# Kernel tuning notes

Measured on AMD Instinct MI355X. Metric: run time of the kernel, lower is better.

## Reference

```python
import jax, jax.numpy as jnp
import numpy as np
from jax import lax

B, H_IMG, W_IMG = 512, 812, 40
HID = 128
NUM_CLASSES = 12
LSTM_IN = 32 * ((W_IMG - 5) // 2 + 1)  # 32 channels * 18 = 576


def setup_inputs() -> dict:
    key = jax.random.key(0)
    ks = jax.random.split(key, 20)
    s = 0.05
    inp = {
        "x": jax.random.normal(ks[0], (B, 1, H_IMG, W_IMG), jnp.float32),
        "conv_w": jax.random.normal(ks[1], (32, 1, 20, 5), jnp.float32) * s,
        "conv_b": jax.random.normal(ks[2], (32,), jnp.float32) * s,
        "Wih0": jax.random.normal(ks[3], (4 * HID, LSTM_IN), jnp.float32) * s,
        "Whh0": jax.random.normal(ks[4], (4 * HID, HID), jnp.float32) * s,
        "bih0": jax.random.normal(ks[5], (4 * HID,), jnp.float32) * s,
        "bhh0": jax.random.normal(ks[6], (4 * HID,), jnp.float32) * s,
        "Wih1": jax.random.normal(ks[7], (4 * HID, HID), jnp.float32) * s,
        "Whh1": jax.random.normal(ks[8], (4 * HID, HID), jnp.float32) * s,
        "bih1": jax.random.normal(ks[9], (4 * HID,), jnp.float32) * s,
        "bhh1": jax.random.normal(ks[10], (4 * HID,), jnp.float32) * s,
        "W_att": jax.random.normal(ks[11], (HID, HID), jnp.float32) * s,
        "b_att": jax.random.normal(ks[12], (HID,), jnp.float32) * s,
        "v_att": jax.random.normal(ks[13], (HID,), jnp.float32) * s,
        "W1": jax.random.normal(ks[14], (64, HID), jnp.float32) * s,
        "b1": jax.random.normal(ks[15], (64,), jnp.float32) * s,
        "W2": jax.random.normal(ks[16], (NUM_CLASSES, 64), jnp.float32) * s,
        "b2": jax.random.normal(ks[17], (NUM_CLASSES,), jnp.float32) * s,
    }
    return inp


def _lstm_layer(seq, Wih, Whh, bih, bhh):
    # seq: (T, B, I); PyTorch gate order i, f, g, o
    T, Bn, _ = seq.shape
    Hd = Whh.shape[1]
    x_proj = jnp.einsum('tbi,gi->tbg', seq, Wih) + bih + bhh  # (T,B,4H)

    def step(carry, xg):
        h, c = carry
        g = xg + h @ Whh.T
        i, f, gg, o = jnp.split(g, 4, axis=-1)
        c = jax.nn.sigmoid(f) * c + jax.nn.sigmoid(i) * jnp.tanh(gg)
        h = jax.nn.sigmoid(o) * jnp.tanh(c)
        return (h, c), h

    init = (jnp.zeros((Bn, Hd), seq.dtype), jnp.zeros((Bn, Hd), seq.dtype))
    _, hs = lax.scan(step, init, x_proj)
    return hs  # (T,B,H)


def _forward(x, conv_w, conv_b, Wih0, Whh0, bih0, bhh0, Wih1, Whh1, bih1, bhh1,
             W_att, b_att, v_att, W1, b1, W2, b2):
    # Conv2d(1->32, k=(20,5), s=(8,2)) + ReLU
    y = lax.conv_general_dilated(x, conv_w, (8, 2), 'VALID',
                                 dimension_numbers=('NCHW', 'OIHW', 'NCHW'))
    y = jax.nn.relu(y + conv_b[None, :, None, None])  # (B,32,T,W')
    b, c, t, w = y.shape
    # permute(0,2,3,1).view(b,t,-1).permute(1,0,2) -> (T,B,W'*32)
    seq = jnp.transpose(y, (2, 0, 3, 1)).reshape(t, b, w * c)
    # 2-layer LSTM (inter-layer dropout=0.2 inactive at eval)
    h1 = _lstm_layer(seq, Wih0, Whh0, bih0, bhh0)
    h2 = _lstm_layer(h1, Wih1, Whh1, bih1, bhh1)
    # additive attention pooling over time
    squish = jnp.tanh(jnp.einsum('tbh,hk->tbk', h2, W_att) + b_att)  # (T,B,H)
    attn = jnp.einsum('tbh,h->tb', squish, v_att)                     # (T,B)
    w_att_n = jax.nn.softmax(attn, axis=0)                            # softmax over T
    pooled = jnp.einsum('tb,tbh->bh', w_att_n, h2)                    # (B,H)
    # dnn1 -> (dropout inactive at eval) -> output
    hdn = pooled @ W1.T + b1
    return hdn @ W2.T + b2  # (B,num_classes)


def reference(x, conv_w, conv_b, Wih0, Whh0, bih0, bhh0, Wih1, Whh1, bih1, bhh1,
              W_att, b_att, v_att, W1, b1, W2, b2):
    return _forward(x, conv_w, conv_b, Wih0, Whh0, bih0, bhh0, Wih1, Whh1,
                    bih1, bhh1, W_att, b_att, v_att, W1, b1, W2, b2)
```

## Files before the change

kernel.cpp:

```cpp
#include <hip/hip_runtime.h>
#include <stdint.h>


#define T_STEPS 100
#define BATCH   512
#define HIDD    128
#define GATES   512
#define LSTMIN  576
#define HIMG    812
#define WIMG    40

typedef __attribute__((ext_vector_type(8))) short bf16x8;
typedef __attribute__((ext_vector_type(4))) float f32x4;
typedef __attribute__((ext_vector_type(2))) __fp16 f16x2;
typedef unsigned long long ull;

__device__ inline unsigned short f2bf(float f) {
  unsigned u = __float_as_uint(f);
  unsigned r = (u + 0x7fffu + ((u >> 16) & 1u)) >> 16;
  return (unsigned short)r;
}
__device__ inline unsigned pk_bf16(float a, float b) {
#if __has_builtin(__builtin_amdgcn_cvt_pk_bf16_f32)
  auto r = __builtin_amdgcn_cvt_pk_bf16_f32(a, b);
  return __builtin_bit_cast(unsigned, r);
#else
  return (unsigned)f2bf(a) | ((unsigned)f2bf(b) << 16);
#endif
}
__device__ inline float bf2f(unsigned short b) {
  return __uint_as_float(((unsigned)b) << 16);
}
__device__ inline float fsigm(float x) {
  float e = __expf(-x);
  return __builtin_amdgcn_rcpf(1.f + e);
}
__device__ inline float ftanh(float x) {
  float e = __expf(2.f * x);
  return (e - 1.f) * __builtin_amdgcn_rcpf(e + 1.f);
}
__device__ inline void lds_barrier() {
  asm volatile("s_waitcnt lgkmcnt(0)" ::: "memory");
  __builtin_amdgcn_s_barrier();
}
__device__ inline void wait_flag(int* fp, int need) {
  if ((threadIdx.x & 63) == 0) {
    while (__hip_atomic_load(fp, __ATOMIC_RELAXED, __HIP_MEMORY_SCOPE_AGENT) < need)
      __builtin_amdgcn_s_sleep(2);
  }
  asm volatile("" ::: "memory");
}

__global__ void prep_kernel(const float* __restrict__ Wih0, const float* __restrict__ Whh0,
                            const float* __restrict__ Wih1, const float* __restrict__ Whh1,
                            const float* __restrict__ Watt, const float* __restrict__ convw,
                            const float* __restrict__ bih0, const float* __restrict__ bhh0,
                            const float* __restrict__ bih1, const float* __restrict__ bhh1,
                            unsigned short* __restrict__ wih0b, unsigned short* __restrict__ whh0b,
                            unsigned short* __restrict__ wih1b, unsigned short* __restrict__ whh1b,
                            unsigned short* __restrict__ wattb, f16x2* __restrict__ wpair,
                            float* __restrict__ bias0, float* __restrict__ bias1,
                            int* __restrict__ flags) {
  int tid = blockIdx.x * blockDim.x + threadIdx.x;
  int stride = gridDim.x * blockDim.x;
  for (int i = tid; i < GATES * LSTMIN; i += stride) wih0b[i] = f2bf(Wih0[i]);
  for (int i = tid; i < GATES * HIDD; i += stride) whh0b[i] = f2bf(Whh0[i]);
  for (int i = tid; i < GATES * HIDD; i += stride) wih1b[i] = f2bf(Wih1[i]);
  for (int i = tid; i < GATES * HIDD; i += stride) whh1b[i] = f2bf(Whh1[i]);
  for (int i = tid; i < HIDD * HIDD; i += stride) {
    int j = i >> 7, k = i & 127;
    wattb[i] = f2bf(Watt[k * HIDD + j]);
  }
  for (int i = tid; i < 50 * 32; i += stride) {
    int k2 = i >> 5, c = i & 31;
    int kh2 = k2 / 5, kw = k2 % 5;
    float lo = convw[c * 100 + (2 * kh2) * 5 + kw];
    float hi = convw[c * 100 + (2 * kh2 + 1) * 5 + kw];
    wpair[i] = __builtin_amdgcn_cvt_pkrtz(lo, hi);
  }
  for (int i = tid; i < GATES; i += stride) bias0[i] = bih0[i] + bhh0[i];
  for (int i = tid; i < GATES; i += stride) bias1[i] = bih1[i] + bhh1[i];
  for (int i = tid; i < 32; i += stride) flags[i] = 0;
}

__global__ __launch_bounds__(256) void conv_kernel(const float* __restrict__ x,
                                                   const f16x2* __restrict__ wpair,
                                                   const float* __restrict__ convb,
                                                   unsigned short* __restrict__ seq) {
  __shared__ f16x2 imgp[106 * WIMG];
  const int b = blockIdx.x;
  const int chunk = blockIdx.y;
  const int t0 = chunk * 25;
  const float* src = x + (size_t)b * (HIMG * WIMG) + (size_t)(8 * t0) * WIMG;
  for (int i = threadIdx.x; i < 106 * WIMG; i += 256) {
    int r2 = i / WIMG, c = i % WIMG;
    float lo = src[(2 * r2) * WIMG + c];
    float hi = src[(2 * r2 + 1) * WIMG + c];
    imgp[i] = __builtin_amdgcn_cvt_pkrtz(lo, hi);
  }
  __syncthreads();
  for (int p = threadIdx.x; p < 450; p += 256) {
    int tl = p / 18, wp = p % 18;
    int t = t0 + tl;
    float acc[32];
#pragma unroll
    for (int c = 0; c < 32; ++c) acc[c] = 0.f;
    const f16x2* ibase = imgp + (4 * tl) * WIMG + 2 * wp;
#pragma unroll 2
    for (int kh2 = 0; kh2 < 10; ++kh2) {
#pragma unroll
      for (int kw = 0; kw < 5; ++kw) {
        f16x2 iv = ibase[kh2 * WIMG + kw];
        const f16x2* wk = wpair + (kh2 * 5 + kw) * 32;
#pragma unroll
        for (int c = 0; c < 32; ++c)
          acc[c] = __builtin_amdgcn_fdot2(iv, wk[c], acc[c], false);
      }
    }
    unsigned short* o = seq + ((size_t)(t * BATCH + b)) * LSTMIN + wp * 32;
#pragma unroll
    for (int c = 0; c < 32; ++c) {
      float v = acc[c] + convb[c];
      o[c] = f2bf(v > 0.f ? v : 0.f);
    }
  }
}

template <int KDIM>
__global__ __launch_bounds__(256) void gemm_xp_kernel(const unsigned short* __restrict__ A,
                                                      const unsigned short* __restrict__ Bw,
                                                      const float* __restrict__ bias,
                                                      unsigned short* __restrict__ Xp) {
  __shared__ __align__(16) unsigned short As[128 * 32];
  __shared__ __align__(16) unsigned short Bs[128 * 32];
  const int tid = threadIdx.x;
  const int lane = tid & 63;
  const int w = tid >> 6;
  const int col16 = lane & 15;
  const int q = lane >> 4;
  const int n0 = blockIdx.x * 128;
  const int m0 = blockIdx.y * 128;
  const int wm = (w & 1) * 64;
  const int wn = (w >> 1) * 64;
  f32x4 acc[4][4] = {};
  const int r = tid >> 2;
  const int sw = ((tid & 3) ^ (r & 3)) * 8;
  const unsigned wslot = (unsigned)w * 512;
  const unsigned short* ga = A + (size_t)(m0 + r) * KDIM + sw;
  const unsigned short* gb = Bw + (size_t)(n0 + r) * KDIM + sw;
  for (int k0 = 0; k0 < KDIM; k0 += 32) {
    __syncthreads();
    __builtin_amdgcn_global_load_lds((const __attribute__((address_space(1))) void*)(ga + k0),
                                     (__attribute__((address_space(3))) void*)(As + wslot), 16, 0, 0);
    __builtin_amdgcn_global_load_lds((const __attribute__((address_space(1))) void*)(ga + k0 + (size_t)64 * KDIM),
                                     (__attribute__((address_space(3))) void*)(As + wslot + 2048), 16, 0, 0);
    __builtin_amdgcn_global_load_lds((const __attribute__((address_space(1))) void*)(gb + k0),
                                     (__attribute__((address_space(3))) void*)(Bs + wslot), 16, 0, 0);
    __builtin_amdgcn_global_load_lds((const __attribute__((address_space(1))) void*)(gb + k0 + (size_t)64 * KDIM),
                                     (__attribute__((address_space(3))) void*)(Bs + wslot + 2048), 16, 0, 0);
    __syncthreads();
    bf16x8 af[4], bv[4];
#pragma unroll
    for (int i = 0; i < 4; ++i) {
      int ra = wm + i * 16 + col16;
      af[i] = *(const bf16x8*)(As + ra * 32 + ((q ^ (ra & 3)) * 8));
      int rb2 = wn + i * 16 + col16;
      bv[i] = *(const bf16x8*)(Bs + rb2 * 32 + ((q ^ (rb2 & 3)) * 8));
    }
#pragma unroll
    for (int i = 0; i < 4; ++i)
#pragma unroll
      for (int j = 0; j < 4; ++j)
        acc[i][j] = __builtin_amdgcn_mfma_f32_16x16x32_bf16(af[i], bv[j], acc[i][j], 0, 0, 0);
  }
#pragma unroll
  for (int ct = 0; ct < 4; ++ct) {
    int n = n0 + wn + ct * 16 + col16;
    float bvv = bias[n];
    int g = n >> 7;
    int rr2 = n & 127;
    int wqS = rr2 >> 5;
    int ntS = g * 2 + ((rr2 >> 4) & 1);
    int c16S = n & 15;
#pragma unroll
    for (int rt = 0; rt < 4; ++rt) {
      int m = m0 + wm + rt * 16 + q * 4;
      int t = m >> 9;
      int bb = m & 511;
      int blkS = bb >> 4;
      int r16 = bb & 15;
      ushort4 u;
      u.x = f2bf(acc[rt][ct][0] + bvv);
      u.y = f2bf(acc[rt][ct][1] + bvv);
      u.z = f2bf(acc[rt][ct][2] + bvv);
      u.w = f2bf(acc[rt][ct][3] + bvv);
      size_t tile = (((size_t)t * 32 + blkS) * 4 + wqS) * 8 + ntS;
      *(ushort4*)(Xp + tile * 256 + c16S * 16 + r16) = u;
    }
  }
}

__global__ __launch_bounds__(512, 2) void scan_pipe_kernel(
    const unsigned short* __restrict__ Xp0, const unsigned short* __restrict__ Whh0,
    const unsigned short* __restrict__ Wih1, const float* __restrict__ bias1,
    unsigned short* __restrict__ Xp1, const unsigned short* __restrict__ Whh1,
    unsigned short* __restrict__ hout, int* __restrict__ flags) {
  __shared__ __align__(16) unsigned short hb[2][16 * 136];
  const int tid = threadIdx.x;
  const int lane = tid & 63;
  const int w = tid >> 6;
  const int wq = w & 3;
  const int role = w >> 2;
  const int col16 = lane & 15;
  const int q = lane >> 4;
  const bool producer = blockIdx.x < 32;
  const int blk = producer ? (int)blockIdx.x : (int)blockIdx.x - 32;
  const int rb = blk * 16;
  int* flagp = flags + blk;
  const size_t TSTRIDE = (size_t)GATES * BATCH;
  const size_t TSTRIDE8 = TSTRIDE / 4;

  {
    unsigned short* hz = (unsigned short*)hb;
    for (int i = tid; i < 2 * 16 * 136; i += 512) hz[i] = 0;
  }

  if (producer) {
    if (role == 0) {
      bf16x8 bfrag[8][4];
      const unsigned short* xpb[8];
#pragma unroll
      for (int nt = 0; nt < 8; ++nt) {
        int cn = (nt >> 1) * HIDD + wq * 32 + (nt & 1) * 16 + col16;
#pragma unroll
        for (int ks = 0; ks < 4; ++ks)
          bfrag[nt][ks] = *(const bf16x8*)(Whh0 + (size_t)cn * HIDD + ks * 32 + q * 8);
        size_t tile = (((size_t)blk) * 4 + wq) * 8 + nt;
        xpb[nt] = Xp0 + tile * 256 + col16 * 16 + q * 4;
      }
      uint2 xb[2][8];
#pragma unroll
      for (int nt = 0; nt < 8; ++nt) xb[0][nt] = *(const uint2*)(xpb[nt]);
#pragma unroll
      for (int nt = 0; nt < 8; ++nt) xb[1][nt] = *(const uint2*)(xpb[nt] + TSTRIDE);
      float cst[8] = {0.f, 0.f, 0.f, 0.f, 0.f, 0.f, 0.f, 0.f};
      lds_barrier();
#pragma unroll 2
      for (int t = 0; t < T_STEPS; ++t) {
        const int s = t & 1;
        uint2 xv[8];
#pragma unroll
        for (int nt = 0; nt < 8; ++nt) xv[nt] = xb[s][nt];
        if (t + 2 < T_STEPS) {
#pragma unroll
          for (int nt = 0; nt < 8; ++nt)
            xb[s][nt] = *(const uint2*)(xpb[nt] + (size_t)(t + 2) * TSTRIDE);
        }
        bf16x8 af[4];
#pragma unroll
        for (int ks = 0; ks < 4; ++ks)
          af[ks] = *(const bf16x8*)(hb[s ^ 1] + col16 * 136 + ks * 32 + q * 8);
        f32x4 acc[8];
#pragma unroll
        for (int nt = 0; nt < 8; ++nt) {
          acc[nt][0] = __uint_as_float(xv[nt].x << 16);
          acc[nt][1] = __uint_as_float(xv[nt].x & 0xffff0000u);
          acc[nt][2] = __uint_as_float(xv[nt].y << 16);
          acc[nt][3] = __uint_as_float(xv[nt].y & 0xffff0000u);
        }
#pragma unroll
        for (int ks = 0; ks < 4; ++ks)
#pragma unroll
          for (int nt = 0; nt < 8; ++nt)
            acc[nt] = __builtin_amdgcn_mfma_f32_16x16x32_bf16(af[ks], bfrag[nt][ks], acc[nt], 0, 0, 0);
#pragma unroll
        for (int hh = 0; hh < 2; ++hh)
#pragma unroll
          for (int rr = 0; rr < 4; ++rr) {
            int idx = hh * 4 + rr;
            float pi = acc[0 + hh][rr];
            float pf = acc[2 + hh][rr];
            float pg = acc[4 + hh][rr];
            float po = acc[6 + hh][rr];
            float cc = fsigm(pf) * cst[idx] + fsigm(pi) * ftanh(pg);
            cst[idx] = cc;
            hb[s][(q * 4 + rr) * 136 + wq * 32 + hh * 16 + col16] = f2bf(fsigm(po) * ftanh(cc));
          }
        lds_barrier();
      }
      lds_barrier();
    } else {
      bf16x8 bfrag2[8][4];
      float biasn[8];
      ull* xob[8];
#pragma unroll
      for (int nt = 0; nt < 8; ++nt) {
        int cn = (nt >> 1) * HIDD + wq * 32 + (nt & 1) * 16 + col16;
#pragma unroll
        for (int ks = 0; ks < 4; ++ks)
          bfrag2[nt][ks] = *(const bf16x8*)(Wih1 + (size_t)cn * HIDD + ks * 32 + q * 8);
        biasn[nt] = bias1[cn];
        size_t tile = (((size_t)blk) * 4 + wq) * 8 + nt;
        xob[nt] = (ull*)(Xp1 + tile * 256 + col16 * 16 + q * 4);
      }
      lds_barrier();
#pragma unroll 2
      for (int t = 0; t < T_STEPS; ++t) {
        const int s = t & 1;
        if (t > 0) {
          bf16x8 af[4];
#pragma unroll
          for (int ks = 0; ks < 4; ++ks)
            af[ks] = *(const bf16x8*)(hb[s ^ 1] + col16 * 136 + ks * 32 + q * 8);
          f32x4 acc2[8];
#pragma unroll
          for (int nt = 0; nt < 8; ++nt) acc2[nt] = f32x4{0.f, 0.f, 0.f, 0.f};
#pragma unroll
          for (int ks = 0; ks < 4; ++ks)
#pragma unroll
            for (int nt = 0; nt < 8; ++nt)
              acc2[nt] = __builtin_amdgcn_mfma_f32_16x16x32_bf16(af[ks], bfrag2[nt][ks], acc2[nt], 0, 0, 0);
#pragma unroll
          for (int nt = 0; nt < 8; ++nt) {
            unsigned lo = pk_bf16(acc2[nt][0] + biasn[nt], acc2[nt][1] + biasn[nt]);
            unsigned hi = pk_bf16(acc2[nt][2] + biasn[nt], acc2[nt][3] + biasn[nt]);
            __hip_atomic_store(xob[nt] + (size_t)(t - 1) * TSTRIDE8,
                               (ull)lo | ((ull)hi << 32),
                               __ATOMIC_RELAXED, __HIP_MEMORY_SCOPE_AGENT);
          }
        }
        if ((t & 3) == 3) {
          asm volatile("s_waitcnt vmcnt(0) lgkmcnt(0)\ns_barrier" ::: "memory");
          if (tid == 256)
            __hip_atomic_store(flagp, t, __ATOMIC_RELAXED, __HIP_MEMORY_SCOPE_AGENT);
        } else {
          lds_barrier();
        }
      }
      {
        bf16x8 af[4];
#pragma unroll
        for (int ks = 0; ks < 4; ++ks)
          af[ks] = *(const bf16x8*)(hb[(T_STEPS - 1) & 1] + col16 * 136 + ks * 32 + q * 8);
        f32x4 acc2[8];
#pragma unroll
        for (int nt = 0; nt < 8; ++nt) acc2[nt] = f32x4{0.f, 0.f, 0.f, 0.f};
#pragma unroll
        for (int ks = 0; ks < 4; ++ks)
#pragma unroll
          for (int nt = 0; nt < 8; ++nt)
            acc2[nt] = __builtin_amdgcn_mfma_f32_16x16x32_bf16(af[ks], bfrag2[nt][ks], acc2[nt], 0, 0, 0);
#pragma unroll
        for (int nt = 0; nt < 8; ++nt) {
          unsigned lo = pk_bf16(acc2[nt][0] + biasn[nt], acc2[nt][1] + biasn[nt]);
          unsigned hi = pk_bf16(acc2[nt][2] + biasn[nt], acc2[nt][3] + biasn[nt]);
          __hip_atomic_store(xob[nt] + (size_t)(T_STEPS - 1) * TSTRIDE8,
                             (ull)lo | ((ull)hi << 32),
                             __ATOMIC_RELAXED, __HIP_MEMORY_SCOPE_AGENT);
        }
        asm volatile("s_waitcnt vmcnt(0) lgkmcnt(0)\ns_barrier" ::: "memory");
        if (tid == 256)
          __hip_atomic_store(flagp, 100, __ATOMIC_RELAXED, __HIP_MEMORY_SCOPE_AGENT);
      }
    }
  } else {
    if (role == 0) {
      bf16x8 bfrag[8][4];
      ull* xpb[8];
#pragma unroll
      for (int nt = 0; nt < 8; ++nt) {
        int cn = (nt >> 1) * HIDD + wq * 32 + (nt & 1) * 16 + col16;
#pragma unroll
        for (int ks = 0; ks < 4; ++ks)
          bfrag[nt][ks] = *(const bf16x8*)(Whh1 + (size_t)cn * HIDD + ks * 32 + q * 8);
        size_t tile = (((size_t)blk) * 4 + wq) * 8 + nt;
        xpb[nt] = (ull*)(Xp1 + tile * 256 + col16 * 16 + q * 4);
      }
      wait_flag(flagp, 6);
      ull xb[2][8];
#pragma unroll
      for (int nt = 0; nt < 8; ++nt)
        xb[0][nt] = __hip_atomic_load(xpb[nt], __ATOMIC_RELAXED, __HIP_MEMORY_SCOPE_AGENT);
#pragma unroll
      for (int nt = 0; nt < 8; ++nt)
        xb[1][nt] = __hip_atomic_load(xpb[nt] + TSTRIDE8, __ATOMIC_RELAXED, __HIP_MEMORY_SCOPE_AGENT);
      float cst[8] = {0.f, 0.f, 0.f, 0.f, 0.f, 0.f, 0.f, 0.f};
      lds_barrier();
#pragma unroll 2
      for (int t = 0; t < T_STEPS; ++t) {
        if (t > 0 && (t & 3) == 0) {
          int need = t + 6;
          if (need > 100) need = 100;
          wait_flag(flagp, need);
        }
        const int s = t & 1;
        ull xv[8];
#pragma unroll
        for (int nt = 0; nt < 8; ++nt) xv[nt] = xb[s][nt];
        if (t + 2 < T_STEPS) {
#pragma unroll
          for (int nt = 0; nt < 8; ++nt)
            xb[s][nt] = __hip_atomic_load(xpb[nt] + (size_t)(t + 2) * TSTRIDE8,
                                          __ATOMIC_RELAXED, __HIP_MEMORY_SCOPE_AGENT);
        }
        bf16x8 af[4];
#pragma unroll
        for (int ks = 0; ks < 4; ++ks)
          af[ks] = *(const bf16x8*)(hb[s ^ 1] + col16 * 136 + ks * 32 + q * 8);
        f32x4 acc[8];
#pragma unroll
        for (int nt = 0; nt < 8; ++nt) {
          unsigned lo = (unsigned)xv[nt];
          unsigned hi = (unsigned)(xv[nt] >> 32);
          acc[nt][0] = __uint_as_float(lo << 16);
          acc[nt][1] = __uint_as_float(lo & 0xffff0000u);
          acc[nt][2] = __uint_as_float(hi << 16);
          acc[nt][3] = __uint_as_float(hi & 0xffff0000u);
        }
#pragma unroll
        for (int ks = 0; ks < 4; ++ks)
#pragma unroll
          for (int nt = 0; nt < 8; ++nt)
            acc[nt] = __builtin_amdgcn_mfma_f32_16x16x32_bf16(af[ks], bfrag[nt][ks], acc[nt], 0, 0, 0);
#pragma unroll
        for (int hh = 0; hh < 2; ++hh)
#pragma unroll
          for (int rr = 0; rr < 4; ++rr) {
            int idx = hh * 4 + rr;
            float pi = acc[0 + hh][rr];
            float pf = acc[2 + hh][rr];
            float pg = acc[4 + hh][rr];
            float po = acc[6 + hh][rr];
            float cc = fsigm(pf) * cst[idx] + fsigm(pi) * ftanh(pg);
            cst[idx] = cc;
            hb[s][(q * 4 + rr) * 136 + wq * 32 + hh * 16 + col16] = f2bf(fsigm(po) * ftanh(cc));
          }
        lds_barrier();
      }
    } else {
      const int c = wq * 64 + lane;
      const int row = c >> 4;
      const int ch = c & 15;
      lds_barrier();
#pragma unroll 2
      for (int t = 0; t < T_STEPS; ++t) {
        if (t > 0) {
          uint4 hx = *(const uint4*)(hb[(t - 1) & 1] + row * 136 + ch * 8);
          *(uint4*)(hout + ((size_t)((t - 1) * BATCH) + rb + row) * HIDD + ch * 8) = hx;
        }
        lds_barrier();
      }
      uint4 hx = *(const uint4*)(hb[(T_STEPS - 1) & 1] + row * 136 + ch * 8);
      *(uint4*)(hout + ((size_t)((T_STEPS - 1) * BATCH) + rb + row) * HIDD + ch * 8) = hx;
    }
  }
}

__global__ __launch_bounds__(256) void gemm_att_kernel(const unsigned short* __restrict__ A,
                                                       const unsigned short* __restrict__ Bw,
                                                       const float* __restrict__ b_att,
                                                       const float* __restrict__ v_att,
                                                       float* __restrict__ scores) {
  __shared__ __align__(16) unsigned short As[128 * 32];
  __shared__ __align__(16) unsigned short Bs[128 * 32];
  __shared__ float s_red[128];
  const int tid = threadIdx.x;
  const int lane = tid & 63;
  const int w = tid >> 6;
  const int col16 = lane & 15;
  const int q = lane >> 4;
  const int m0 = blockIdx.y * 128;
  const int wm = (w & 1) * 64;
  const int wn = (w >> 1) * 64;
  f32x4 acc[4][4] = {};
  const int r = tid >> 2;
  const int sw = ((tid & 3) ^ (r & 3)) * 8;
  const unsigned wslot = (unsigned)w * 512;
  const unsigned short* ga = A + (size_t)(m0 + r) * HIDD + sw;
  const unsigned short* gb = Bw + (size_t)r * HIDD + sw;
  for (int k0 = 0; k0 < HIDD; k0 += 32) {
    __syncthreads();
    __builtin_amdgcn_global_load_lds((const __attribute__((address_space(1))) void*)(ga + k0),
                                     (__attribute__((address_space(3))) void*)(As + wslot), 16, 0, 0);
    __builtin_amdgcn_global_load_lds((const __attribute__((address_space(1))) void*)(ga + k0 + (size_t)64 * HIDD),
                                     (__attribute__((address_space(3))) void*)(As + wslot + 2048), 16, 0, 0);
    __builtin_amdgcn_global_load_lds((const __attribute__((address_space(1))) void*)(gb + k0),
                                     (__attribute__((address_space(3))) void*)(Bs + wslot), 16, 0, 0);
    __builtin_amdgcn_global_load_lds((const __attribute__((address_space(1))) void*)(gb + k0 + (size_t)64 * HIDD),
                                     (__attribute__((address_space(3))) void*)(Bs + wslot + 2048), 16, 0, 0);
    __syncthreads();
    bf16x8 af[4], bv[4];
#pragma unroll
    for (int i = 0; i < 4; ++i) {
      int ra = wm + i * 16 + col16;
      af[i] = *(const bf16x8*)(As + ra * 32 + ((q ^ (ra & 3)) * 8));
      int rb2 = wn + i * 16 + col16;
      bv[i] = *(const bf16x8*)(Bs + rb2 * 32 + ((q ^ (rb2 & 3)) * 8));
    }
#pragma unroll
    for (int i = 0; i < 4; ++i)
#pragma unroll
      for (int j = 0; j < 4; ++j)
        acc[i][j] = __builtin_amdgcn_mfma_f32_16x16x32_bf16(af[i], bv[j], acc[i][j], 0, 0, 0);
  }
  if (tid < 128) s_red[tid] = 0.f;
  float rs[4][4];
#pragma unroll
  for (int rt = 0; rt < 4; ++rt)
#pragma unroll
    for (int rr = 0; rr < 4; ++rr) rs[rt][rr] = 0.f;
#pragma unroll
  for (int ct = 0; ct < 4; ++ct) {
    int n = wn + ct * 16 + col16;
    float bvv = b_att[n], vv = v_att[n];
#pragma unroll
    for (int rt = 0; rt < 4; ++rt)
#pragma unroll
      for (int rr = 0; rr < 4; ++rr) {
        float xv2 = acc[rt][ct][rr] + bvv;
        float e = __expf(2.f * xv2);
        rs[rt][rr] += vv * (e - 1.f) * __builtin_amdgcn_rcpf(e + 1.f);
      }
  }
#pragma unroll
  for (int off = 1; off < 16; off <<= 1)
#pragma unroll
    for (int rt = 0; rt < 4; ++rt)
#pragma unroll
      for (int rr = 0; rr < 4; ++rr) rs[rt][rr] += __shfl_xor(rs[rt][rr], off, 64);
  __syncthreads();
  if (col16 == 0) {
#pragma unroll
    for (int rt = 0; rt < 4; ++rt)
#pragma unroll
      for (int rr = 0; rr < 4; ++rr)
        atomicAdd(&s_red[wm + rt * 16 + q * 4 + rr], rs[rt][rr]);
  }
  __syncthreads();
  if (tid < 128) scores[m0 + tid] = s_red[tid];
}

__global__ __launch_bounds__(128) void final_kernel(const float* __restrict__ scores,
                                                    const unsigned short* __restrict__ h2,
                                                    const float* __restrict__ W1, const float* __restrict__ b1,
                                                    const float* __restrict__ W2, const float* __restrict__ b2,
                                                    float* __restrict__ out) {
  const int b = blockIdx.x;
  const int tid = threadIdx.x;
  __shared__ float wj[T_STEPS];
  __shared__ float red[128];
  __shared__ float pooled[128];
  __shared__ float hdn[64];
  float sv = (tid < T_STEPS) ? scores[tid * BATCH + b] : -1e30f;
  red[tid] = sv;
  __syncthreads();
#pragma unroll
  for (int off = 64; off > 0; off >>= 1) {
    if (tid < off) red[tid] = fmaxf(red[tid], red[tid + off]);
    __syncthreads();
  }
  float mx = red[0];
  __syncthreads();
  float ev = (tid < T_STEPS) ? __expf(sv - mx) : 0.f;
  red[tid] = ev;
  __syncthreads();
#pragma unroll
  for (int off = 64; off > 0; off >>= 1) {
    if (tid < off) red[tid] += red[tid + off];
    __syncthreads();
  }
  float inv = 1.0f / red[0];
  if (tid < T_STEPS) wj[tid] = ev * inv;
  __syncthreads();
  float p = 0.f;
#pragma unroll 4
  for (int t = 0; t < T_STEPS; ++t)
    p += wj[t] * bf2f(h2[((size_t)(t * BATCH + b)) * HIDD + tid]);
  pooled[tid] = p;
  __syncthreads();
  if (tid < 64) {
    float a = b1[tid];
    for (int h = 0; h < 128; ++h) a = fmaf(W1[tid * 128 + h], pooled[h], a);
    hdn[tid] = a;
  }
  __syncthreads();
  if (tid < 12) {
    float a = b2[tid];
    for (int j = 0; j < 64; ++j) a = fmaf(W2[tid * 64 + j], hdn[j], a);
    out[b * 12 + tid] = a;
  }
}

extern "C" void kernel_launch(void* const* d_in, const int* in_sizes, int n_in,
                              void* d_out, int out_size, void* d_ws, size_t ws_size,
                              hipStream_t stream) {
  (void)in_sizes; (void)n_in; (void)out_size; (void)ws_size;
  const float* x      = (const float*)d_in[0];
  const float* conv_w = (const float*)d_in[1];
  const float* conv_b = (const float*)d_in[2];
  const float* Wih0   = (const float*)d_in[3];
  const float* Whh0   = (const float*)d_in[4];
  const float* bih0   = (const float*)d_in[5];
  const float* bhh0   = (const float*)d_in[6];
  const float* Wih1   = (const float*)d_in[7];
  const float* Whh1   = (const float*)d_in[8];
  const float* bih1   = (const float*)d_in[9];
  const float* bhh1   = (const float*)d_in[10];
  const float* W_att  = (const float*)d_in[11];
  const float* b_att  = (const float*)d_in[12];
  const float* v_att  = (const float*)d_in[13];
  const float* W1     = (const float*)d_in[14];
  const float* b1     = (const float*)d_in[15];
  const float* W2     = (const float*)d_in[16];
  const float* b2     = (const float*)d_in[17];

  char* ws = (char*)d_ws;
  size_t off = 0;
  auto carve = [&](size_t bytes) { char* p = ws + off; off += (bytes + 255) & ~(size_t)255; return p; };
  unsigned short* seq    = (unsigned short*)carve((size_t)T_STEPS * BATCH * LSTMIN * 2);
  unsigned short* xp0    = (unsigned short*)carve((size_t)T_STEPS * GATES * BATCH * 2);
  unsigned short* h2     = (unsigned short*)carve((size_t)T_STEPS * BATCH * HIDD * 2);
  float*          scores = (float*)carve((size_t)T_STEPS * BATCH * 4);
  unsigned short* wih0b  = (unsigned short*)carve((size_t)GATES * LSTMIN * 2);
  unsigned short* whh0b  = (unsigned short*)carve((size_t)GATES * HIDD * 2);
  unsigned short* wih1b  = (unsigned short*)carve((size_t)GATES * HIDD * 2);
  unsigned short* whh1b  = (unsigned short*)carve((size_t)GATES * HIDD * 2);
  unsigned short* wattb  = (unsigned short*)carve((size_t)HIDD * HIDD * 2);
  f16x2*          wpair  = (f16x2*)carve(50 * 32 * 4);
  float*          bias0  = (float*)carve(GATES * 4);
  float*          bias1  = (float*)carve(GATES * 4);
  int*            flags  = (int*)carve(32 * 4);
  unsigned short* xp1 = seq;

  prep_kernel<<<256, 256, 0, stream>>>(Wih0, Whh0, Wih1, Whh1, W_att, conv_w,
                                       bih0, bhh0, bih1, bhh1,
                                       wih0b, whh0b, wih1b, whh1b, wattb, wpair,
                                       bias0, bias1, flags);
  conv_kernel<<<dim3(512, 4), 256, 0, stream>>>(x, wpair, conv_b, seq);
  gemm_xp_kernel<LSTMIN><<<dim3(4, 400), 256, 0, stream>>>(seq, wih0b, bias0, xp0);
  scan_pipe_kernel<<<64, 512, 0, stream>>>(xp0, whh0b, wih1b, bias1, xp1, whh1b, h2, flags);
  gemm_att_kernel<<<dim3(1, 400), 256, 0, stream>>>(h2, wattb, b_att, v_att, scores);
  final_kernel<<<512, 128, 0, stream>>>(scores, h2, W1, b1, W2, b2, (float*)d_out);
}
```

Measured before the change: 421.1 us.

## Fuse input-projection GEMM into scan kernel with per-timestep readiness flags

Merges the layer-0 input projection GEMM and the two-layer LSTM scan into one launch. Blocks 0-63 run the scan as before, and blocks 64+ compute GEMM tiles, then bump a per-timestep counter that the layer-0 producer polls before consuming Xp0 for upcoming steps. The aim is to overlap the large GEMM with the serial recurrence and drop one launch boundary. The design relies on the scan blocks being scheduled ahead of the GEMM blocks, since they spin on flags. GEMM blocks now share one B tile between two 128-row halves, and the scan's LDS footprint grows, which risks lower occupancy or contention on the scan's critical path.

```diff
diff --git a/kernel.cpp b/kernel.cpp
--- a/kernel.cpp
+++ b/kernel.cpp
@@ -47,6 +47,14 @@
   if ((threadIdx.x & 63) == 0) {
     while (__hip_atomic_load(fp, __ATOMIC_RELAXED, __HIP_MEMORY_SCOPE_AGENT) < need)
       __builtin_amdgcn_s_sleep(2);
+  }
+  asm volatile("" ::: "memory");
+}
+__device__ inline void wait_gemm(int* gf, int lo, int hi) {
+  if ((threadIdx.x & 63) == 0) {
+    for (int j = lo; j <= hi; ++j)
+      while (__hip_atomic_load(gf + j, __ATOMIC_RELAXED, __HIP_MEMORY_SCOPE_AGENT) < 8)
+        __builtin_amdgcn_s_sleep(2);
   }
   asm volatile("" ::: "memory");
 }
@@ -80,7 +88,7 @@
   }
   for (int i = tid; i < GATES; i += stride) bias0[i] = bih0[i] + bhh0[i];
   for (int i = tid; i < GATES; i += stride) bias1[i] = bih1[i] + bhh1[i];
-  for (int i = tid; i < 32; i += stride) flags[i] = 0;
+  for (int i = tid; i < 132; i += stride) flags[i] = 0;
 }
 
 __global__ __launch_bounds__(256) void conv_kernel(const float* __restrict__ x,
@@ -126,104 +134,111 @@
   }
 }
 
-template <int KDIM>
-__global__ __launch_bounds__(256) void gemm_xp_kernel(const unsigned short* __restrict__ A,
-                                                      const unsigned short* __restrict__ Bw,
-                                                      const float* __restrict__ bias,
-                                                      unsigned short* __restrict__ Xp) {
-  __shared__ __align__(16) unsigned short As[128 * 32];
-  __shared__ __align__(16) unsigned short Bs[128 * 32];
+__global__ __launch_bounds__(512) void mega_kernel(
+    const unsigned short* __restrict__ seq, const unsigned short* __restrict__ Wih0b,
+    const float* __restrict__ bias0, unsigned short* __restrict__ Xp0,
+    const unsigned short* __restrict__ Whh0, const unsigned short* __restrict__ Wih1,
+    const float* __restrict__ bias1, unsigned short* __restrict__ Xp1,
+    const unsigned short* __restrict__ Whh1, unsigned short* __restrict__ hout,
+    int* __restrict__ flags) {
+  __shared__ __align__(16) unsigned short hb_s[2 * 2176];
+  __shared__ __align__(16) unsigned short As_s[2][4096];
+  __shared__ __align__(16) unsigned short Bs_s[4096];
   const int tid = threadIdx.x;
-  const int lane = tid & 63;
-  const int w = tid >> 6;
-  const int col16 = lane & 15;
-  const int q = lane >> 4;
-  const int n0 = blockIdx.x * 128;
-  const int m0 = blockIdx.y * 128;
-  const int wm = (w & 1) * 64;
-  const int wn = (w >> 1) * 64;
-  f32x4 acc[4][4] = {};
-  const int r = tid >> 2;
-  const int sw = ((tid & 3) ^ (r & 3)) * 8;
-  const unsigned wslot = (unsigned)w * 512;
-  const unsigned short* ga = A + (size_t)(m0 + r) * KDIM + sw;
-  const unsigned short* gb = Bw + (size_t)(n0 + r) * KDIM + sw;
-  for (int k0 = 0; k0 < KDIM; k0 += 32) {
+  const int bid = blockIdx.x;
+  const size_t TSTRIDE = (size_t)GATES * BATCH;
+  const size_t TSTRIDE8 = TSTRIDE / 4;
+  int* gflag = flags + 32;
+
+  if (bid >= 64) {
+    const int g = bid - 64;
+    const int mp = g >> 2;
+    const int nb = g & 3;
+    const int half = tid >> 8;
+    const int t256 = tid & 255;
+    const int m0 = mp * 256 + half * 128;
+    const int n0 = nb * 128;
+    const int tt = mp >> 1;
+    unsigned short* As = As_s[half];
+    const int lane = t256 & 63;
+    const int w4 = t256 >> 6;
+    const int col16 = lane & 15;
+    const int q = lane >> 4;
+    const int wm = (w4 & 1) * 64;
+    const int wn = (w4 >> 1) * 64;
+    f32x4 acc[4][4] = {};
+    const int r = t256 >> 2;
+    const int sw = ((t256 & 3) ^ (r & 3)) * 8;
+    const unsigned wslot = (unsigned)w4 * 512;
+    const unsigned short* ga = seq + (size_t)(m0 + r) * LSTMIN + sw;
+    const unsigned short* gb = Wih0b + (size_t)(n0 + r) * LSTMIN + sw;
+    for (int k0 = 0; k0 < LSTMIN; k0 += 32) {
+      __syncthreads();
+      __builtin_amdgcn_global_load_lds((const __attribute__((address_space(1))) void*)(ga + k0),
+                                       (__attribute__((address_space(3))) void*)(As + wslot), 16, 0, 0);
+      __builtin_amdgcn_global_load_lds((const __attribute__((address_space(1))) void*)(ga + k0 + (size_t)64 * LSTMIN),
+                                       (__attribute__((address_space(3))) void*)(As + wslot + 2048), 16, 0, 0);
+      if (half == 0) {
+        __builtin_amdgcn_global_load_lds((const __attribute__((address_space(1))) void*)(gb + k0),
+                                         (__attribute__((address_space(3))) void*)(Bs_s + wslot), 16, 0, 0);
+        __builtin_amdgcn_global_load_lds((const __attribute__((address_space(1))) void*)(gb + k0 + (size_t)64 * LSTMIN),
+                                         (__attribute__((address_space(3))) void*)(Bs_s + wslot + 2048), 16, 0, 0);
+      }
+      __syncthreads();
+      bf16x8 af[4], bv[4];
+#pragma unroll
+      for (int i = 0; i < 4; ++i) {
+        int ra = wm + i * 16 + col16;
+        af[i] = *(const bf16x8*)(As + ra * 32 + ((q ^ (ra & 3)) * 8));
+        int rb2 = wn + i * 16 + col16;
+        bv[i] = *(const bf16x8*)(Bs_s + rb2 * 32 + ((q ^ (rb2 & 3)) * 8));
+      }
+#pragma unroll
+      for (int i = 0; i < 4; ++i)
+#pragma unroll
+        for (int j = 0; j < 4; ++j)
+          acc[i][j] = __builtin_amdgcn_mfma_f32_16x16x32_bf16(af[i], bv[j], acc[i][j], 0, 0, 0);
+    }
+#pragma unroll
+    for (int ct = 0; ct < 4; ++ct) {
+      int n = n0 + wn + ct * 16 + col16;
+      float bvv = bias0[n];
+      int g2 = n >> 7, rr2 = n & 127;
+      int wqS = rr2 >> 5, ntS = g2 * 2 + ((rr2 >> 4) & 1), c16S = n & 15;
+#pragma unroll
+      for (int rt = 0; rt < 4; ++rt) {
+        int m = m0 + wm + rt * 16 + q * 4;
+        int bb = m & 511;
+        int blkS = bb >> 4, r16 = bb & 15;
+        unsigned lo = pk_bf16(acc[rt][ct][0] + bvv, acc[rt][ct][1] + bvv);
+        unsigned hi = pk_bf16(acc[rt][ct][2] + bvv, acc[rt][ct][3] + bvv);
+        size_t tile = (((size_t)tt * 32 + blkS) * 4 + wqS) * 8 + ntS;
+        __hip_atomic_store((ull*)(Xp0 + tile * 256 + c16S * 16 + r16),
+                           (ull)lo | ((ull)hi << 32),
+                           __ATOMIC_RELAXED, __HIP_MEMORY_SCOPE_AGENT);
+      }
+    }
+    asm volatile("s_waitcnt vmcnt(0) lgkmcnt(0)" ::: "memory");
     __syncthreads();
-    __builtin_amdgcn_global_load_lds((const __attribute__((address_space(1))) void*)(ga + k0),
-                                     (__attribute__((address_space(3))) void*)(As + wslot), 16, 0, 0);
-    __builtin_amdgcn_global_load_lds((const __attribute__((address_space(1))) void*)(ga + k0 + (size_t)64 * KDIM),
-                                     (__attribute__((address_space(3))) void*)(As + wslot + 2048), 16, 0, 0);
-    __builtin_amdgcn_global_load_lds((const __attribute__((address_space(1))) void*)(gb + k0),
-                                     (__attribute__((address_space(3))) void*)(Bs + wslot), 16, 0, 0);
-    __builtin_amdgcn_global_load_lds((const __attribute__((address_space(1))) void*)(gb + k0 + (size_t)64 * KDIM),
-                                     (__attribute__((address_space(3))) void*)(Bs + wslot + 2048), 16, 0, 0);
-    __syncthreads();
-    bf16x8 af[4], bv[4];
-#pragma unroll
-    for (int i = 0; i < 4; ++i) {
-      int ra = wm + i * 16 + col16;
-      af[i] = *(const bf16x8*)(As + ra * 32 + ((q ^ (ra & 3)) * 8));
-      int rb2 = wn + i * 16 + col16;
-      bv[i] = *(const bf16x8*)(Bs + rb2 * 32 + ((q ^ (rb2 & 3)) * 8));
-    }
-#pragma unroll
-    for (int i = 0; i < 4; ++i)
-#pragma unroll
-      for (int j = 0; j < 4; ++j)
-        acc[i][j] = __builtin_amdgcn_mfma_f32_16x16x32_bf16(af[i], bv[j], acc[i][j], 0, 0, 0);
-  }
-#pragma unroll
-  for (int ct = 0; ct < 4; ++ct) {
-    int n = n0 + wn + ct * 16 + col16;
-    float bvv = bias[n];
-    int g = n >> 7;
-    int rr2 = n & 127;
-    int wqS = rr2 >> 5;
-    int ntS = g * 2 + ((rr2 >> 4) & 1);
-    int c16S = n & 15;
-#pragma unroll
-    for (int rt = 0; rt < 4; ++rt) {
-      int m = m0 + wm + rt * 16 + q * 4;
-      int t = m >> 9;
-      int bb = m & 511;
-      int blkS = bb >> 4;
-      int r16 = bb & 15;
-      ushort4 u;
-      u.x = f2bf(acc[rt][ct][0] + bvv);
-      u.y = f2bf(acc[rt][ct][1] + bvv);
-      u.z = f2bf(acc[rt][ct][2] + bvv);
-      u.w = f2bf(acc[rt][ct][3] + bvv);
-      size_t tile = (((size_t)t * 32 + blkS) * 4 + wqS) * 8 + ntS;
-      *(ushort4*)(Xp + tile * 256 + c16S * 16 + r16) = u;
-    }
-  }
-}
-
-__global__ __launch_bounds__(512, 2) void scan_pipe_kernel(
-    const unsigned short* __restrict__ Xp0, const unsigned short* __restrict__ Whh0,
-    const unsigned short* __restrict__ Wih1, const float* __restrict__ bias1,
-    unsigned short* __restrict__ Xp1, const unsigned short* __restrict__ Whh1,
-    unsigned short* __restrict__ hout, int* __restrict__ flags) {
-  __shared__ __align__(16) unsigned short hb[2][16 * 136];
-  const int tid = threadIdx.x;
+    if (tid == 0)
+      __hip_atomic_fetch_add(gflag + tt, 1, __ATOMIC_RELAXED, __HIP_MEMORY_SCOPE_AGENT);
+    return;
+  }
+
   const int lane = tid & 63;
   const int w = tid >> 6;
   const int wq = w & 3;
   const int role = w >> 2;
   const int col16 = lane & 15;
   const int q = lane >> 4;
-  const bool producer = blockIdx.x < 32;
-  const int blk = producer ? (int)blockIdx.x : (int)blockIdx.x - 32;
+  const bool producer = bid < 32;
+  const int blk = producer ? bid : bid - 32;
   const int rb = blk * 16;
   int* flagp = flags + blk;
-  const size_t TSTRIDE = (size_t)GATES * BATCH;
-  const size_t TSTRIDE8 = TSTRIDE / 4;
-
-  {
-    unsigned short* hz = (unsigned short*)hb;
-    for (int i = tid; i < 2 * 16 * 136; i += 512) hz[i] = 0;
-  }
+  unsigned short* hb0 = hb_s;
+  unsigned short* hb1 = hb_s + 2176;
+
+  for (int i = tid; i < 2 * 2176; i += 512) hb_s[i] = 0;
 
   if (producer) {
     if (role == 0) {
@@ -238,6 +253,7 @@
         size_t tile = (((size_t)blk) * 4 + wq) * 8 + nt;
         xpb[nt] = Xp0 + tile * 256 + col16 * 16 + q * 4;
       }
+      wait_gemm(gflag, 0, 1);
       uint2 xb[2][8];
 #pragma unroll
       for (int nt = 0; nt < 8; ++nt) xb[0][nt] = *(const uint2*)(xpb[nt]);
@@ -247,7 +263,13 @@
       lds_barrier();
 #pragma unroll 2
       for (int t = 0; t < T_STEPS; ++t) {
+        if ((t & 3) == 0) {
+          int hi = t + 5; if (hi > 99) hi = 99;
+          wait_gemm(gflag, t + 2, hi);
+        }
         const int s = t & 1;
+        unsigned short* hw = s ? hb1 : hb0;
+        unsigned short* hr = s ? hb0 : hb1;
         uint2 xv[8];
 #pragma unroll
         for (int nt = 0; nt < 8; ++nt) xv[nt] = xb[s][nt];
@@ -259,7 +281,7 @@
         bf16x8 af[4];
 #pragma unroll
         for (int ks = 0; ks < 4; ++ks)
-          af[ks] = *(const bf16x8*)(hb[s ^ 1] + col16 * 136 + ks * 32 + q * 8);
+          af[ks] = *(const bf16x8*)(hr + col16 * 136 + ks * 32 + q * 8);
         f32x4 acc[8];
 #pragma unroll
         for (int nt = 0; nt < 8; ++nt) {
@@ -284,7 +306,7 @@
             float po = acc[6 + hh][rr];
             float cc = fsigm(pf) * cst[idx] + fsigm(pi) * ftanh(pg);
             cst[idx] = cc;
-            hb[s][(q * 4 + rr) * 136 + wq * 32 + hh * 16 + col16] = f2bf(fsigm(po) * ftanh(cc));
+            hw[(q * 4 + rr) * 136 + wq * 32 + hh * 16 + col16] = f2bf(fsigm(po) * ftanh(cc));
           }
         lds_barrier();
       }
@@ -307,11 +329,12 @@
 #pragma unroll 2
       for (int t = 0; t < T_STEPS; ++t) {
         const int s = t & 1;
+        unsigned short* hr = s ? hb0 : hb1;
         if (t > 0) {
           bf16x8 af[4];
 #pragma unroll
           for (int ks = 0; ks < 4; ++ks)
-            af[ks] = *(const bf16x8*)(hb[s ^ 1] + col16 * 136 + ks * 32 + q * 8);
+            af[ks] = *(const bf16x8*)(hr + col16 * 136 + ks * 32 + q * 8);
           f32x4 acc2[8];
 #pragma unroll
           for (int nt = 0; nt < 8; ++nt) acc2[nt] = f32x4{0.f, 0.f, 0.f, 0.f};
@@ -338,10 +361,11 @@
         }
       }
       {
+        unsigned short* hr = ((T_STEPS - 1) & 1) ? hb1 : hb0;
         bf16x8 af[4];
 #pragma unroll
         for (int ks = 0; ks < 4; ++ks)
-          af[ks] = *(const bf16x8*)(hb[(T_STEPS - 1) & 1] + col16 * 136 + ks * 32 + q * 8);
+          af[ks] = *(const bf16x8*)(hr + col16 * 136 + ks * 32 + q * 8);
         f32x4 acc2[8];
 #pragma unroll
         for (int nt = 0; nt < 8; ++nt) acc2[nt] = f32x4{0.f, 0.f, 0.f, 0.f};
@@ -394,6 +418,8 @@
           wait_flag(flagp, need);
         }
         const int s = t & 1;
+        unsigned short* hw = s ? hb1 : hb0;
+        unsigned short* hr = s ? hb0 : hb1;
         ull xv[8];
 #pragma unroll
         for (int nt = 0; nt < 8; ++nt) xv[nt] = xb[s][nt];
@@ -406,7 +432,7 @@
         bf16x8 af[4];
 #pragma unroll
         for (int ks = 0; ks < 4; ++ks)
-          af[ks] = *(const bf16x8*)(hb[s ^ 1] + col16 * 136 + ks * 32 + q * 8);
+          af[ks] = *(const bf16x8*)(hr + col16 * 136 + ks * 32 + q * 8);
         f32x4 acc[8];
 #pragma unroll
         for (int nt = 0; nt < 8; ++nt) {
@@ -433,7 +459,7 @@
             float po = acc[6 + hh][rr];
             float cc = fsigm(pf) * cst[idx] + fsigm(pi) * ftanh(pg);
             cst[idx] = cc;
-            hb[s][(q * 4 + rr) * 136 + wq * 32 + hh * 16 + col16] = f2bf(fsigm(po) * ftanh(cc));
+            hw[(q * 4 + rr) * 136 + wq * 32 + hh * 16 + col16] = f2bf(fsigm(po) * ftanh(cc));
           }
         lds_barrier();
       }
@@ -445,12 +471,14 @@
 #pragma unroll 2
       for (int t = 0; t < T_STEPS; ++t) {
         if (t > 0) {
-          uint4 hx = *(const uint4*)(hb[(t - 1) & 1] + row * 136 + ch * 8);
+          unsigned short* hr = ((t - 1) & 1) ? hb1 : hb0;
+          uint4 hx = *(const uint4*)(hr + row * 136 + ch * 8);
           *(uint4*)(hout + ((size_t)((t - 1) * BATCH) + rb + row) * HIDD + ch * 8) = hx;
         }
         lds_barrier();
       }
-      uint4 hx = *(const uint4*)(hb[(T_STEPS - 1) & 1] + row * 136 + ch * 8);
+      unsigned short* hr = ((T_STEPS - 1) & 1) ? hb1 : hb0;
+      uint4 hx = *(const uint4*)(hr + row * 136 + ch * 8);
       *(uint4*)(hout + ((size_t)((T_STEPS - 1) * BATCH) + rb + row) * HIDD + ch * 8) = hx;
     }
   }
@@ -629,7 +657,7 @@
   f16x2*          wpair  = (f16x2*)carve(50 * 32 * 4);
   float*          bias0  = (float*)carve(GATES * 4);
   float*          bias1  = (float*)carve(GATES * 4);
-  int*            flags  = (int*)carve(32 * 4);
+  int*            flags  = (int*)carve(132 * 4);
   unsigned short* xp1 = seq;
 
   prep_kernel<<<256, 256, 0, stream>>>(Wih0, Whh0, Wih1, Whh1, W_att, conv_w,
@@ -637,8 +665,8 @@
                                        wih0b, whh0b, wih1b, whh1b, wattb, wpair,
                                        bias0, bias1, flags);
   conv_kernel<<<dim3(512, 4), 256, 0, stream>>>(x, wpair, conv_b, seq);
-  gemm_xp_kernel<LSTMIN><<<dim3(4, 400), 256, 0, stream>>>(seq, wih0b, bias0, xp0);
-  scan_pipe_kernel<<<64, 512, 0, stream>>>(xp0, whh0b, wih1b, bias1, xp1, whh1b, h2, flags);
+  mega_kernel<<<864, 512, 0, stream>>>(seq, wih0b, bias0, xp0,
+                                       whh0b, wih1b, bias1, xp1, whh1b, h2, flags);
   gemm_att_kernel<<<dim3(1, 400), 256, 0, stream>>>(h2, wattb, b_att, v_att, scores);
   final_kernel<<<512, 128, 0, stream>>>(scores, h2, W1, b1, W2, b2, (float*)d_out);
 }
```

Measured after the change: 419.5 us. Within noise of the previous version (-0.4%).
